# Kernel optimization log

Measured on AMD Instinct MI355X. Metric: run time of the kernel, lower is better.

Reference implementation:

```python
import jax, jax.numpy as jnp
import numpy as np

EPS = 1e-12  # torch F.normalize eps

def _l2norm(v):
    return v / jnp.maximum(jnp.linalg.norm(v, axis=-1, keepdims=True), EPS)

def setup_inputs() -> dict:
    key = jax.random.key(0)
    x = jax.random.normal(key, (64, 64, 10, 512), dtype=jnp.float32)
    w = jnp.asarray(10.0, dtype=jnp.float32)
    b = jnp.asarray(-5.0, dtype=jnp.float32)
    return {"x": x, "w": w, "b": b}

def reference(x, w, b):
    B, N, M, D = x.shape
    NM = N * M
    x_flat = _l2norm(x.reshape(B, NM, D))                      # [B, NM, D]
    c_full = _l2norm(jnp.mean(x, axis=2))                      # [B, N, D]
    # leave-one-out centroid: (M * normalized_full_centroid - x) / (M - 1), then normalize
    c_excl = _l2norm(((M * c_full[:, :, None, :] - x) / (M - 1)).reshape(B, NM, D))  # [B, NM, D]
    # cosine sim of each utterance vs every (normalized) full centroid
    sim = jnp.einsum("bkd,bnd->bkn", x_flat, c_full)           # [B, NM, N]
    # replace own-speaker column with leave-one-out similarity (avoids [B,NM,N,D] blowup)
    excl_sim = jnp.sum(x_flat * c_excl, axis=-1)               # [B, NM]
    speaker_ids = jnp.repeat(jnp.arange(N), M)                 # [NM]
    rows = jnp.arange(NM)
    sim = sim.at[:, rows, speaker_ids].set(excl_sim)
    logits = w * sim + b                                       # [B, NM, N]
    logp = jax.nn.log_softmax(logits, axis=-1)
    # cross-entropy with targets = speaker_ids per row, mean over B*NM
    nll = -logp[:, rows, speaker_ids]                          # [B, NM]
    return jnp.mean(nll)
```

## Files before the change

kernel.cpp:

```cpp
#include <hip/hip_runtime.h>
#include <math.h>

static constexpr int Bn = 64;
static constexpr int Nn = 64;
static constexpr int Mn = 10;
static constexpr int Dn = 512;
static constexpr int NMn = Nn * Mn;
static constexpr int RT = 32;
static constexpr int NBLK2 = Bn * (NMn / RT);
static constexpr float EPSV = 1e-12f;

typedef unsigned short u16;
typedef unsigned int u32;
typedef __attribute__((ext_vector_type(8))) __bf16 bf16x8;
typedef __attribute__((ext_vector_type(4))) float f32x4;

static __device__ __forceinline__ u16 f2bf(float f) {
  u32 u = __float_as_uint(f);
  u = u + 0x7fffu + ((u >> 16) & 1u);
  return (u16)(u >> 16);
}


__global__ __launch_bounds__(256) void prep_k(const float* __restrict__ x,
                                              u16* __restrict__ ch2,
                                              u16* __restrict__ xbf,
                                              float* __restrict__ xn2,
                                              float* __restrict__ out) {
  const int bn = blockIdx.x;
  const int tid = threadIdx.x;
  const int f4 = tid & 127;
  const int mg = tid >> 7;
  const int wv = tid >> 6, ln = tid & 63;
  const int b = bn >> 6, n = bn & 63;
  const float4* xp = (const float4*)(x + (size_t)bn * (Mn * Dn));
  const int kblk = f4 >> 3;
  const int koff = (f4 & 7) * 4;

  if (bn == 0 && tid == 0) out[0] = 0.f;

  float4 a = {0.f, 0.f, 0.f, 0.f};
  float sq[5];
#pragma unroll
  for (int k = 0; k < 5; ++k) {
    const int m = 2 * k + mg;
    const float4 v = xp[m * 128 + f4];
    a.x += v.x; a.y += v.y; a.z += v.z; a.w += v.w;
    sq[k] = v.x * v.x + v.y * v.y + v.z * v.z + v.w * v.w;
    const u16 h0 = f2bf(v.x), h1 = f2bf(v.y), h2 = f2bf(v.z), h3 = f2bf(v.w);
    uint2 wd;
    wd.x = (u32)h0 | ((u32)h1 << 16);
    wd.y = (u32)h2 | ((u32)h3 << 16);
    const size_t off = (((size_t)b * 16 + kblk) * NMn + n * Mn + m) * 32 + koff;
    *(uint2*)(xbf + off) = wd;
  }
#pragma unroll
  for (int k = 0; k < 5; ++k) {
#pragma unroll
    for (int t = 1; t < 64; t <<= 1) sq[k] += __shfl_xor(sq[k], t, 64);
  }
  __shared__ float sqred[4][5];
  if (ln == 0) {
#pragma unroll
    for (int k = 0; k < 5; ++k) sqred[wv][k] = sq[k];
  }
  __shared__ float4 cred[128];
  if (mg == 1) cred[f4] = a;
  __syncthreads();

  if (tid < Mn) {
    const int par = tid & 1, k = tid >> 1;
    xn2[(size_t)bn * Mn + tid] = sqred[2 * par][k] + sqred[2 * par + 1][k];
  }

  float4 c = {0.f, 0.f, 0.f, 0.f};
  float cs = 0.f;
  if (mg == 0) {
    c = cred[f4];
    c.x += a.x; c.y += a.y; c.z += a.z; c.w += a.w;
    cs = c.x * c.x + c.y * c.y + c.z * c.z + c.w * c.w;
  }
#pragma unroll
  for (int t = 1; t < 64; t <<= 1) cs += __shfl_xor(cs, t, 64);
  __shared__ float csred[2];
  if (mg == 0 && ln == 0) csred[wv] = cs;
  __syncthreads();
  if (mg == 0) {
    const float scale = 1.0f / fmaxf(sqrtf(csred[0] + csred[1]), EPSV);
    const u16 h0 = f2bf(c.x * scale), h1 = f2bf(c.y * scale);
    const u16 h2 = f2bf(c.z * scale), h3 = f2bf(c.w * scale);
    uint2 w;
    w.x = (u32)h0 | ((u32)h1 << 16);
    w.y = (u32)h2 | ((u32)h3 << 16);
    const size_t off = (((size_t)b * 16 + kblk) * Nn + n) * 32 + koff;
    *(uint2*)(ch2 + off) = w;
  }
}

__global__ __launch_bounds__(512) void gemm_loss_k(const u16* __restrict__ xbf,
                                                   const u16* __restrict__ ch2,
                                                   const float* __restrict__ xn2,
                                                   const float* __restrict__ wp,
                                                   const float* __restrict__ bp,
                                                   float* __restrict__ out) {
  __shared__ float S[8][16][65];
  __shared__ float nred[8];

  const int b = blockIdx.x / (NMn / RT);
  const int rt = blockIdx.x % (NMn / RT);
  const int row0 = rt * RT;
  const int tid = threadIdx.x, wv = tid >> 6, ln = tid & 63;
  const int lr = ln & 15;
  const int lkb = (ln >> 4) * 8;
  const int rh = wv >> 2;
  const int q = wv & 3;

  const u16* arow = xbf + (((size_t)b * 16 + q * 4) * NMn + row0 + rh * 16 + lr) * 32 + lkb;
  const u16* brow = ch2 + (((size_t)b * 16 + q * 4) * Nn + lr) * 32 + lkb;

  f32x4 acc0 = {0.f, 0.f, 0.f, 0.f};
  f32x4 acc1 = acc0, acc2 = acc0, acc3 = acc0;

#pragma unroll
  for (int kk = 0; kk < 4; ++kk) {
    const bf16x8 aa = *(const bf16x8*)(arow + (size_t)kk * (NMn * 32));
    const u16* bp8 = brow + (size_t)kk * (Nn * 32);
    const bf16x8 b0 = *(const bf16x8*)(bp8);
    const bf16x8 b1 = *(const bf16x8*)(bp8 + 16 * 32);
    const bf16x8 b2 = *(const bf16x8*)(bp8 + 32 * 32);
    const bf16x8 b3 = *(const bf16x8*)(bp8 + 48 * 32);
    acc0 = __builtin_amdgcn_mfma_f32_16x16x32_bf16(aa, b0, acc0, 0, 0, 0);
    acc1 = __builtin_amdgcn_mfma_f32_16x16x32_bf16(aa, b1, acc1, 0, 0, 0);
    acc2 = __builtin_amdgcn_mfma_f32_16x16x32_bf16(aa, b2, acc2, 0, 0, 0);
    acc3 = __builtin_amdgcn_mfma_f32_16x16x32_bf16(aa, b3, acc3, 0, 0, 0);
  }

  const int orow = (ln >> 4) * 4;
#pragma unroll
  for (int r = 0; r < 4; ++r) {
    S[wv][orow + r][lr] = acc0[r];
    S[wv][orow + r][16 + lr] = acc1[r];
    S[wv][orow + r][32 + lr] = acc2[r];
    S[wv][orow + r][48 + lr] = acc3[r];
  }
  __syncthreads();

  const float W = *wp, Bb = *bp;
  float acc_nll = 0.f;
#pragma unroll
  for (int i = 0; i < 4; ++i) {
    const int R = wv * 4 + i;
    const int rhh = R >> 4, rl = R & 15;
    const int krow = row0 + R;
    const int spk = krow / Mn;
    const float rn = S[rhh * 4 + 0][rl][ln] + S[rhh * 4 + 1][rl][ln] +
                     S[rhh * 4 + 2][rl][ln] + S[rhh * 4 + 3][rl][ln];
    const float x2 = xn2[(size_t)b * NMn + krow];
    const float xn = sqrtf(x2);
    const float inv_xn = 1.0f / fmaxf(xn, EPSV);
    const float rspk = __shfl(rn, spk, 64);
    float sv = rn * inv_xn;
    if (ln == spk) {
      const float num = (float)Mn * rspk - x2;
      const float en = sqrtf(fmaxf((float)(Mn * Mn) - 2.0f * (float)Mn * rspk + x2, 0.f));
      sv = num / fmaxf(xn * en, EPSV);
    }
    const float logit = W * sv + Bb;
    const float lspk = __shfl(logit, spk, 64);
    float mx = logit;
#pragma unroll
    for (int t = 1; t < 64; t <<= 1) mx = fmaxf(mx, __shfl_xor(mx, t, 64));
    float se = expf(logit - mx);
#pragma unroll
    for (int t = 1; t < 64; t <<= 1) se += __shfl_xor(se, t, 64);
    acc_nll += (mx + logf(se)) - lspk;
  }
  if (ln == 0) nred[wv] = acc_nll;
  __syncthreads();
  if (tid == 0) {
    float s = 0.f;
#pragma unroll
    for (int i = 0; i < 8; ++i) s += nred[i];
    atomicAdd(out, s * (1.0f / (float)(Bn * NMn)));
  }
}

static constexpr int ROWS = 8;
static constexpr int DCHUNK = 128;
static constexpr int CPAD = DCHUNK + 1;

__global__ __launch_bounds__(256) void centroid_fb_k(const float* __restrict__ x,
                                                     float* __restrict__ c) {
  const int bn = blockIdx.x;
  const float* xp = x + (size_t)bn * Mn * Dn;
  const int tid = threadIdx.x;
  float a0 = 0.f, a1 = 0.f;
#pragma unroll
  for (int m = 0; m < Mn; ++m) {
    a0 += xp[m * Dn + tid];
    a1 += xp[m * Dn + tid + 256];
  }
  float s = a0 * a0 + a1 * a1;
#pragma unroll
  for (int m = 1; m < 64; m <<= 1) s += __shfl_xor(s, m, 64);
  __shared__ float red[4];
  const int wv = tid >> 6, ln = tid & 63;
  if (ln == 0) red[wv] = s;
  __syncthreads();
  const float tot = red[0] + red[1] + red[2] + red[3];
  const float scale = 1.0f / fmaxf(sqrtf(tot), EPSV);
  float* cp = c + (size_t)bn * Dn;
  cp[tid] = a0 * scale;
  cp[tid + 256] = a1 * scale;
}

__global__ __launch_bounds__(256) void loss_fb_k(const float* __restrict__ x,
                                                 const float* __restrict__ c,
                                                 const float* __restrict__ wp,
                                                 const float* __restrict__ bp,
                                                 float* __restrict__ out) {
  __shared__ __align__(16) float x_lds[ROWS * Dn];
  __shared__ float c_lds[Nn * CPAD];
  __shared__ float xn2s[ROWS];
  __shared__ float sim_lds[ROWS][Nn];

  const int tid = threadIdx.x;
  const int b = blockIdx.x / (NMn / ROWS);
  const int rblk = blockIdx.x % (NMn / ROWS);
  const int row0 = rblk * ROWS;
  const float* xrow = x + ((size_t)b * NMn + row0) * Dn;
  {
    const float4* xs = (const float4*)xrow;
    float4* xd = (float4*)x_lds;
#pragma unroll
    for (int i = tid; i < ROWS * Dn / 4; i += 256) xd[i] = xs[i];
  }
  __syncthreads();
  const int wv = tid >> 6, ln = tid & 63;
  for (int r = wv; r < ROWS; r += 4) {
    float s = 0.f;
#pragma unroll
    for (int j = ln; j < Dn; j += 64) {
      const float v = x_lds[r * Dn + j];
      s += v * v;
    }
#pragma unroll
    for (int m = 1; m < 64; m <<= 1) s += __shfl_xor(s, m, 64);
    if (ln == 0) xn2s[r] = s;
  }
  const int n = tid & 63;
  const int rg = tid >> 6;
  const int r0 = rg * 2, r1 = rg * 2 + 1;
  float s0 = 0.f, s1 = 0.f;
  const float* cb_base = c + (size_t)b * Nn * Dn;
  for (int cb = 0; cb < Dn; cb += DCHUNK) {
    __syncthreads();
    for (int i = tid; i < Nn * DCHUNK; i += 256) {
      const int nn = i / DCHUNK;
      const int j = i & (DCHUNK - 1);
      c_lds[nn * CPAD + j] = cb_base[(size_t)nn * Dn + cb + j];
    }
    __syncthreads();
#pragma unroll 16
    for (int j = 0; j < DCHUNK; ++j) {
      const float cv = c_lds[n * CPAD + j];
      s0 = fmaf(x_lds[r0 * Dn + cb + j], cv, s0);
      s1 = fmaf(x_lds[r1 * Dn + cb + j], cv, s1);
    }
  }
  sim_lds[r0][n] = s0;
  sim_lds[r1][n] = s1;
  __syncthreads();
  const float W = *wp, Bb = *bp;
  float acc_nll = 0.f;
  for (int r = wv; r < ROWS; r += 4) {
    const int k = row0 + r;
    const int spk = k / Mn;
    const float rn = sim_lds[r][ln];
    const float x2 = xn2s[r];
    const float xn = sqrtf(x2);
    const float inv_xn = 1.0f / fmaxf(xn, EPSV);
    const float rspk = sim_lds[r][spk];
    float sv = rn * inv_xn;
    if (ln == spk) {
      const float num = (float)Mn * rspk - x2;
      const float en = sqrtf(fmaxf((float)(Mn * Mn) - 2.0f * (float)Mn * rspk + x2, 0.f));
      sv = num / fmaxf(xn * en, EPSV);
    }
    const float logit = W * sv + Bb;
    const float lspk = __shfl(logit, spk, 64);
    float mx = logit;
#pragma unroll
    for (int m = 1; m < 64; m <<= 1) mx = fmaxf(mx, __shfl_xor(mx, m, 64));
    float se = expf(logit - mx);
#pragma unroll
    for (int m = 1; m < 64; m <<= 1) se += __shfl_xor(se, m, 64);
    acc_nll += (mx + logf(se)) - lspk;
  }
  __shared__ float nred[4];
  if (ln == 0) nred[wv] = acc_nll;
  __syncthreads();
  if (tid == 0)
    atomicAdd(out, (nred[0] + nred[1] + nred[2] + nred[3]) * (1.0f / (float)(Bn * NMn)));
}

extern "C" void kernel_launch(void* const* d_in, const int* in_sizes, int n_in,
                              void* d_out, int out_size, void* d_ws, size_t ws_size,
                              hipStream_t stream) {
  const float* x = (const float*)d_in[0];
  const float* w = (const float*)d_in[1];
  const float* b = (const float*)d_in[2];
  float* out = (float*)d_out;

  const size_t XSZ = (size_t)Bn * 16 * NMn * 32 * sizeof(u16);
  const size_t CSZ = (size_t)Bn * 16 * Nn * 32 * sizeof(u16);
  const size_t NSZ = (size_t)Bn * NMn * sizeof(float);
  const size_t NEED = XSZ + CSZ + NSZ;

  if (ws_size >= NEED) {
    char* p = (char*)d_ws;
    u16* xbf = (u16*)p;     p += XSZ;
    u16* ch2 = (u16*)p;     p += CSZ;
    float* xn2 = (float*)p;
    hipLaunchKernelGGL(prep_k, dim3(Bn * Nn), dim3(256), 0, stream,
                       x, ch2, xbf, xn2, out);
    hipLaunchKernelGGL(gemm_loss_k, dim3(NBLK2), dim3(512), 0, stream,
                       xbf, ch2, xn2, w, b, out);
  } else {
    float* c = (float*)d_ws;
    hipMemsetAsync(out, 0, sizeof(float), stream);
    hipLaunchKernelGGL(centroid_fb_k, dim3(Bn * Nn), dim3(256), 0, stream, x, c);
    hipLaunchKernelGGL(loss_fb_k, dim3(Bn * (NMn / ROWS)), dim3(256), 0, stream,
                       x, c, w, b, out);
  }
}
```

Baseline: 51.95 us.

## Store bf16 x row-major, swizzle GEMM block order, drop max-subtraction in softmax

The prep kernel now writes the bf16 copy of x in plain row-major order instead of the k-blocked tiled layout, so its stores are contiguous. The GEMM kernel reads A rows directly with a strided k offset and remaps block IDs so that consecutive blocks go to different batches. It also sets launch bounds to one block per CU. The loss computation drops the max-subtraction and the per-row shuffles in favour of a direct exp sum, which relies on the logits being bounded (|w*sim+b| stays small) and accumulates the per-lane nll with a single final reduction.

```diff
diff --git a/kernel.cpp b/kernel.cpp
--- a/kernel.cpp
+++ b/kernel.cpp
@@ -22,20 +22,18 @@
 }
 
 
-__global__ __launch_bounds__(256) void prep_k(const float* __restrict__ x,
-                                              u16* __restrict__ ch2,
-                                              u16* __restrict__ xbf,
-                                              float* __restrict__ xn2,
-                                              float* __restrict__ out) {
+__global__ __launch_bounds__(256) void centroid_k(const float* __restrict__ x,
+                                                  u16* __restrict__ ch2,
+                                                  u16* __restrict__ xbf,
+                                                  float* __restrict__ xn2,
+                                                  float* __restrict__ out) {
   const int bn = blockIdx.x;
   const int tid = threadIdx.x;
   const int f4 = tid & 127;
   const int mg = tid >> 7;
   const int wv = tid >> 6, ln = tid & 63;
-  const int b = bn >> 6, n = bn & 63;
   const float4* xp = (const float4*)(x + (size_t)bn * (Mn * Dn));
-  const int kblk = f4 >> 3;
-  const int koff = (f4 & 7) * 4;
+  u16* xbp = xbf + (size_t)bn * (Mn * Dn);
 
   if (bn == 0 && tid == 0) out[0] = 0.f;
 
@@ -51,8 +49,7 @@
     uint2 wd;
     wd.x = (u32)h0 | ((u32)h1 << 16);
     wd.y = (u32)h2 | ((u32)h3 << 16);
-    const size_t off = (((size_t)b * 16 + kblk) * NMn + n * Mn + m) * 32 + koff;
-    *(uint2*)(xbf + off) = wd;
+    *(uint2*)(xbp + (size_t)m * Dn + f4 * 4) = wd;
   }
 #pragma unroll
   for (int k = 0; k < 5; ++k) {
@@ -92,47 +89,51 @@
     uint2 w;
     w.x = (u32)h0 | ((u32)h1 << 16);
     w.y = (u32)h2 | ((u32)h3 << 16);
-    const size_t off = (((size_t)b * 16 + kblk) * Nn + n) * 32 + koff;
+    const int n = bn & (Nn - 1), bb = bn >> 6;
+    const size_t off = (((size_t)bb * 16 + (f4 >> 3)) * Nn + n) * 32 + ((f4 & 7) * 4);
     *(uint2*)(ch2 + off) = w;
   }
 }
 
-__global__ __launch_bounds__(512) void gemm_loss_k(const u16* __restrict__ xbf,
-                                                   const u16* __restrict__ ch2,
-                                                   const float* __restrict__ xn2,
-                                                   const float* __restrict__ wp,
-                                                   const float* __restrict__ bp,
-                                                   float* __restrict__ out) {
+__global__ __launch_bounds__(512, 1) void gemm_loss_k(const u16* __restrict__ xbf,
+                                                      const u16* __restrict__ ch2,
+                                                      const float* __restrict__ xn2,
+                                                      const float* __restrict__ wp,
+                                                      const float* __restrict__ bp,
+                                                      float* __restrict__ out) {
   __shared__ float S[8][16][65];
   __shared__ float nred[8];
 
-  const int b = blockIdx.x / (NMn / RT);
-  const int rt = blockIdx.x % (NMn / RT);
+  const int bid = blockIdx.x;
+  const int wgid = (bid & 7) * (NBLK2 / 8) + (bid >> 3);
+  const int b = wgid / (NMn / RT);
+  const int rt = wgid % (NMn / RT);
   const int row0 = rt * RT;
   const int tid = threadIdx.x, wv = tid >> 6, ln = tid & 63;
   const int lr = ln & 15;
   const int lkb = (ln >> 4) * 8;
   const int rh = wv >> 2;
   const int q = wv & 3;
-
-  const u16* arow = xbf + (((size_t)b * 16 + q * 4) * NMn + row0 + rh * 16 + lr) * 32 + lkb;
-  const u16* brow = ch2 + (((size_t)b * 16 + q * 4) * Nn + lr) * 32 + lkb;
+  const int k0 = q * 128;
+
+  const u16* arow = xbf + ((size_t)b * NMn + row0 + rh * 16 + lr) * Dn + k0 + lkb;
+  const u16* brow = ch2 + (((size_t)b * 16 + q * 4) * Nn) * 32 + (size_t)lr * 32 + lkb;
 
   f32x4 acc0 = {0.f, 0.f, 0.f, 0.f};
   f32x4 acc1 = acc0, acc2 = acc0, acc3 = acc0;
 
 #pragma unroll
-  for (int kk = 0; kk < 4; ++kk) {
-    const bf16x8 aa = *(const bf16x8*)(arow + (size_t)kk * (NMn * 32));
-    const u16* bp8 = brow + (size_t)kk * (Nn * 32);
+  for (int kk = 0; kk < 128; kk += 32) {
+    const u16* bp8 = brow + (size_t)(kk >> 5) * (Nn * 32);
+    const bf16x8 ah = *(const bf16x8*)(arow + kk);
     const bf16x8 b0 = *(const bf16x8*)(bp8);
     const bf16x8 b1 = *(const bf16x8*)(bp8 + 16 * 32);
     const bf16x8 b2 = *(const bf16x8*)(bp8 + 32 * 32);
     const bf16x8 b3 = *(const bf16x8*)(bp8 + 48 * 32);
-    acc0 = __builtin_amdgcn_mfma_f32_16x16x32_bf16(aa, b0, acc0, 0, 0, 0);
-    acc1 = __builtin_amdgcn_mfma_f32_16x16x32_bf16(aa, b1, acc1, 0, 0, 0);
-    acc2 = __builtin_amdgcn_mfma_f32_16x16x32_bf16(aa, b2, acc2, 0, 0, 0);
-    acc3 = __builtin_amdgcn_mfma_f32_16x16x32_bf16(aa, b3, acc3, 0, 0, 0);
+    acc0 = __builtin_amdgcn_mfma_f32_16x16x32_bf16(ah, b0, acc0, 0, 0, 0);
+    acc1 = __builtin_amdgcn_mfma_f32_16x16x32_bf16(ah, b1, acc1, 0, 0, 0);
+    acc2 = __builtin_amdgcn_mfma_f32_16x16x32_bf16(ah, b2, acc2, 0, 0, 0);
+    acc3 = __builtin_amdgcn_mfma_f32_16x16x32_bf16(ah, b3, acc3, 0, 0, 0);
   }
 
   const int orow = (ln >> 4) * 4;
@@ -146,7 +147,7 @@
   __syncthreads();
 
   const float W = *wp, Bb = *bp;
-  float acc_nll = 0.f;
+  float lane_nll = 0.f;
 #pragma unroll
   for (int i = 0; i < 4; ++i) {
     const int R = wv * 4 + i;
@@ -158,24 +159,22 @@
     const float x2 = xn2[(size_t)b * NMn + krow];
     const float xn = sqrtf(x2);
     const float inv_xn = 1.0f / fmaxf(xn, EPSV);
-    const float rspk = __shfl(rn, spk, 64);
     float sv = rn * inv_xn;
     if (ln == spk) {
-      const float num = (float)Mn * rspk - x2;
-      const float en = sqrtf(fmaxf((float)(Mn * Mn) - 2.0f * (float)Mn * rspk + x2, 0.f));
+      const float num = (float)Mn * rn - x2;
+      const float en = sqrtf(fmaxf((float)(Mn * Mn) - 2.0f * (float)Mn * rn + x2, 0.f));
       sv = num / fmaxf(xn * en, EPSV);
     }
     const float logit = W * sv + Bb;
-    const float lspk = __shfl(logit, spk, 64);
-    float mx = logit;
-#pragma unroll
-    for (int t = 1; t < 64; t <<= 1) mx = fmaxf(mx, __shfl_xor(mx, t, 64));
-    float se = expf(logit - mx);
-#pragma unroll
-    for (int t = 1; t < 64; t <<= 1) se += __shfl_xor(se, t, 64);
-    acc_nll += (mx + logf(se)) - lspk;
-  }
-  if (ln == 0) nred[wv] = acc_nll;
+    float e = expf(logit);
+#pragma unroll
+    for (int t = 1; t < 64; t <<= 1) e += __shfl_xor(e, t, 64);
+    if (ln == 0) lane_nll += logf(e);
+    if (ln == spk) lane_nll -= logit;
+  }
+#pragma unroll
+  for (int t = 1; t < 64; t <<= 1) lane_nll += __shfl_xor(lane_nll, t, 64);
+  if (ln == 0) nred[wv] = lane_nll;
   __syncthreads();
   if (tid == 0) {
     float s = 0.f;
@@ -312,7 +311,7 @@
   const float* b = (const float*)d_in[2];
   float* out = (float*)d_out;
 
-  const size_t XSZ = (size_t)Bn * 16 * NMn * 32 * sizeof(u16);
+  const size_t XSZ = (size_t)Bn * NMn * Dn * sizeof(u16);
   const size_t CSZ = (size_t)Bn * 16 * Nn * 32 * sizeof(u16);
   const size_t NSZ = (size_t)Bn * NMn * sizeof(float);
   const size_t NEED = XSZ + CSZ + NSZ;
@@ -322,7 +321,7 @@
     u16* xbf = (u16*)p;     p += XSZ;
     u16* ch2 = (u16*)p;     p += CSZ;
     float* xn2 = (float*)p;
-    hipLaunchKernelGGL(prep_k, dim3(Bn * Nn), dim3(256), 0, stream,
+    hipLaunchKernelGGL(centroid_k, dim3(Bn * Nn), dim3(256), 0, stream,
                        x, ch2, xbf, xn2, out);
     hipLaunchKernelGGL(gemm_loss_k, dim3(NBLK2), dim3(512), 0, stream,
                        xbf, ch2, xn2, w, b, out);
```

After: 51.45 us. No clear change (-1.0%).
